# Kernel optimization log

Measured on AMD Instinct MI355X. Metric: run time of the kernel, lower is better.

The kernel has to match this reference:

```python
import jax, jax.numpy as jnp
import numpy as np

# 8 sign-flip operations: all combinations of (+-1, +-1, +-1), shape [8, 3]
OPS = jnp.array([[i, j, k] for i in (-1, 1) for j in (-1, 1) for k in (-1, 1)],
                dtype=jnp.float32)


def setup_inputs() -> dict:
    key = jax.random.key(0)
    k1, k2 = jax.random.split(key)
    B, N = 256, 4096
    X = jax.random.normal(k1, (B, N, 3), dtype=jnp.float32)
    mask = jnp.ones((B, N), dtype=jnp.float32)
    return {"X": X, "mask": mask}


def reference(X, mask):
    # X: [B, N, 3], mask: [B, N]
    m = mask[..., None]                                   # [B, N, 1]
    center = (X * m).sum(axis=1) / m.sum(axis=1)          # [B, 3]
    # torch: X = X - center.unsqueeze(1) * mask  (subtract center only where masked)
    Xc = X - center[:, None, :] * m                       # [B, N, 3]
    # 3x3 covariance per batch element
    C = jnp.einsum('bpi,bpj->bij', Xc, Xc)                # [B, 3, 3]
    # eigh on detached covariance (no grad through eigendecomposition)
    L, V = jnp.linalg.eigh(jax.lax.stop_gradient(C))      # V: [B, 3, 3]
    # F_ops[b,o,i,j] = ops[o,j] * V[b,i,j]  -> [B, 8, 3, 3]
    F_ops = OPS[None, :, None, :] * V[:, None, :, :]
    # h[b,o,p,i] = sum_j F_ops[b,o,j,i] * Xc[b,p,j]
    h = jnp.einsum('boji,bpj->bopi', F_ops, Xc)           # [B, 8, N, 3]
    h = h.reshape(X.shape[0] * 8, X.shape[1], 3)          # [B*8, N, 3]
    return h, jax.lax.stop_gradient(F_ops), center
```

## Files before the change

kernel.cpp:

```cpp
#include <hip/hip_runtime.h>
#include <math.h>

#ifndef USE_NEW_LARTG
#define USE_NEW_LARTG 1
#endif

#define BB 256
#define NN 4096


__device__ __forceinline__ float ssign_(float a, float b) {
  return (b >= 0.0f) ? fabsf(a) : -fabsf(a);
}

__device__ __forceinline__ float slapy2f_(float x, float y) {
#pragma clang fp contract(off)
  float xa = fabsf(x), ya = fabsf(y);
  float w = fmaxf(xa, ya), z = fminf(xa, ya);
  if (z == 0.0f) return w;
  float q = z / w;
  return w * __fsqrt_rn(1.0f + q * q);
}

__device__ __forceinline__ void slartgf_(float f, float g, float& cs, float& sn, float& r) {
#pragma clang fp contract(off)
#if USE_NEW_LARTG
  if (g == 0.0f) { cs = 1.0f; sn = 0.0f; r = f; }
  else if (f == 0.0f) { cs = 0.0f; sn = (g >= 0.0f) ? 1.0f : -1.0f; r = fabsf(g); }
  else {
    float d = __fsqrt_rn(f * f + g * g);
    cs = fabsf(f) / d;
    r = ssign_(d, f);
    sn = g / r;
  }
#else
  if (g == 0.0f) { cs = 1.0f; sn = 0.0f; r = f; }
  else if (f == 0.0f) { cs = 0.0f; sn = 1.0f; r = g; }
  else {
    float rr = __fsqrt_rn(f * f + g * g);
    cs = f / rr; sn = g / rr; r = rr;
    if (fabsf(f) > fabsf(g) && cs < 0.0f) { cs = -cs; sn = -sn; r = -r; }
  }
#endif
}

__device__ __forceinline__ void slaev2f_(float a, float b, float c, float& rt1, float& rt2,
                                         float& cs1, float& sn1) {
#pragma clang fp contract(off)
  float sm = a + c;
  float df = a - c;
  float adf = fabsf(df);
  float tb = b + b;
  float ab = fabsf(tb);
  float acmx, acmn;
  if (fabsf(a) > fabsf(c)) { acmx = a; acmn = c; } else { acmx = c; acmn = a; }
  float rt;
  if (adf > ab)      { float q = ab / adf; rt = adf * __fsqrt_rn(1.0f + q * q); }
  else if (adf < ab) { float q = adf / ab; rt = ab * __fsqrt_rn(1.0f + q * q); }
  else               { rt = ab * __fsqrt_rn(2.0f); }
  int sgn1;
  if (sm < 0.0f)      { rt1 = 0.5f * (sm - rt); sgn1 = -1; rt2 = (acmx / rt1) * acmn - (b / rt1) * b; }
  else if (sm > 0.0f) { rt1 = 0.5f * (sm + rt); sgn1 = 1;  rt2 = (acmx / rt1) * acmn - (b / rt1) * b; }
  else                { rt1 = 0.5f * rt; rt2 = -0.5f * rt; sgn1 = 1; }
  float cs;
  int sgn2;
  if (df >= 0.0f) { cs = df + rt; sgn2 = 1; } else { cs = df - rt; sgn2 = -1; }
  float acs = fabsf(cs);
  if (acs > ab) {
    float ct = -tb / cs;
    sn1 = 1.0f / __fsqrt_rn(1.0f + ct * ct);
    cs1 = ct * sn1;
  } else {
    if (ab == 0.0f) { cs1 = 1.0f; sn1 = 0.0f; }
    else { float tn = -cs / tb; cs1 = 1.0f / __fsqrt_rn(1.0f + tn * tn); sn1 = tn * cs1; }
  }
  if (sgn1 == sgn2) { float tn = cs1; cs1 = -sn1; sn1 = tn; }
}

#define DGET(i)   ((i) == 1 ? d1 : ((i) == 2 ? d2 : d3))
#define DSET(i,v) do { float _t = (v); int _i = (i); \
  d1 = (_i == 1) ? _t : d1; d2 = (_i == 2) ? _t : d2; d3 = (_i == 3) ? _t : d3; } while (0)
#define EGET(i)   ((i) == 1 ? e1 : e2)
#define ESET(i,v) do { float _t = (v); int _i = (i); \
  e1 = (_i == 1) ? _t : e1; e2 = (_i == 2) ? _t : e2; } while (0)
#define WCGET(i)  ((i) == 1 ? wc1 : wc2)
#define WSGET(i)  ((i) == 1 ? ws1 : ws2)
#define WCSET(i,v) do { float _t = (v); int _i = (i); \
  wc1 = (_i == 1) ? _t : wc1; wc2 = (_i == 2) ? _t : wc2; } while (0)
#define WSSET(i,v) do { float _t = (v); int _i = (i); \
  ws1 = (_i == 1) ? _t : ws1; ws2 = (_i == 2) ? _t : ws2; } while (0)
#define ZGETR(rr,j) ((j) == 1 ? z##rr##1 : ((j) == 2 ? z##rr##2 : z##rr##3))
#define ZSETR(rr,j,v) do { float _zv = (v); int _zj = (j); \
  z##rr##1 = (_zj == 1) ? _zv : z##rr##1; \
  z##rr##2 = (_zj == 2) ? _zv : z##rr##2; \
  z##rr##3 = (_zj == 3) ? _zv : z##rr##3; } while (0)
#define ROTR(rr, hi, lo, cc, ss) do { \
  float _zh = ZGETR(rr, (hi)); float _zl = ZGETR(rr, (lo)); \
  float _nh = (cc) * _zh - (ss) * _zl; \
  float _nl = (ss) * _zh + (cc) * _zl; \
  ZSETR(rr, (hi), _nh); ZSETR(rr, (lo), _nl); } while (0)
#define ROTCOLS(hi, lo, cc, ss) do { \
  ROTR(1, hi, lo, cc, ss); ROTR(2, hi, lo, cc, ss); ROTR(3, hi, lo, cc, ss); } while (0)
#define ZSWAPR(rr, i_, k_) do { \
  float _ta = ZGETR(rr, (i_)); float _tb = ZGETR(rr, (k_)); \
  ZSETR(rr, (i_), _tb); ZSETR(rr, (k_), _ta); } while (0)

__device__ __forceinline__ void eigh3_reg(const float C[3][3], float V[3][3]) {
#pragma clang fp contract(off)
  const float eps = 5.9604645e-08f;
  const float eps2 = eps * eps;
  const float safmin = 1.17549435e-38f;
  const int nmaxit = 90;

  float a11 = C[0][0], a21 = C[1][0], a31 = C[2][0];
  float a22 = C[1][1], a32 = C[2][1], a33 = C[2][2];
  float d1, d2, d3, e1, e2, tau1, v3;
  float z11, z12, z13, z21, z22, z23, z31, z32, z33;
  float wc1 = 0.0f, wc2 = 0.0f, ws1 = 0.0f, ws2 = 0.0f;
  int jtot = 0, l1 = 1;
  int m, l, lend, lsv, lendsv, i, j, k, ii;
  float p, g, r, c, s, f, b, rt1, rt2, tst, anorm, cj, sj;

  float xnorm = fabsf(a31);
  if (xnorm == 0.0f) {
    tau1 = 0.0f; v3 = 0.0f;
    d1 = a11; d2 = a22; d3 = a33; e1 = a21; e2 = a32;
  } else {
    float beta = -ssign_(slapy2f_(a21, xnorm), a21);
    tau1 = (beta - a21) / beta;
    v3 = a31 / (a21 - beta);
    e1 = beta;
    float x1 = tau1 * a22 + tau1 * (a32 * v3);
    float x2 = tau1 * a32 + (tau1 * v3) * a33;
    float al = -0.5f * tau1 * (x1 + x2 * v3);
    float w1 = x1 + al;
    float w2 = x2 + al * v3;
    d1 = a11;
    d2 = (a22 - w1) - w1;
    e2 = (a32 - v3 * w1) - w2;
    d3 = (a33 - v3 * w2) - w2 * v3;
  }
  z11 = 1.0f; z12 = 0.0f; z13 = 0.0f;
  z21 = 0.0f; z22 = 1.0f; z23 = 0.0f;
  z31 = 0.0f; z32 = 0.0f; z33 = 1.0f;

L10:
  if (l1 > 3) goto L160;
  if (l1 > 1) ESET(l1 - 1, 0.0f);
  if (l1 <= 2) {
    for (int mm = l1; mm <= 2; ++mm) {
      tst = fabsf(EGET(mm));
      if (tst == 0.0f) { m = mm; goto L30; }
      if (tst <= (__fsqrt_rn(fabsf(DGET(mm))) * __fsqrt_rn(fabsf(DGET(mm + 1)))) * eps) {
        ESET(mm, 0.0f); m = mm; goto L30;
      }
    }
  }
  m = 3;
L30:
  l = l1; lsv = l; lend = m; lendsv = lend; l1 = m + 1;
  if (lend == l) goto L10;
  anorm = 0.0f;
  for (i = l; i <= lend; ++i) anorm = fmaxf(anorm, fabsf(DGET(i)));
  for (i = l; i <= lend - 1; ++i) anorm = fmaxf(anorm, fabsf(EGET(i)));
  if (anorm == 0.0f) goto L10;
  if (fabsf(DGET(lend)) < fabsf(DGET(l))) { lend = lsv; l = lendsv; }

  if (lend > l) {
L40:
    if (l != lend) {
      for (int mm = l; mm <= lend - 1; ++mm) {
        tst = EGET(mm) * EGET(mm);
        if (tst <= (eps2 * fabsf(DGET(mm))) * fabsf(DGET(mm + 1)) + safmin) { m = mm; goto L60; }
      }
    }
    m = lend;
L60:
    if (m < lend) ESET(m, 0.0f);
    p = DGET(l);
    if (m == l) goto L80;
    if (m == l + 1) {
      slaev2f_(DGET(l), EGET(l), DGET(l + 1), rt1, rt2, c, s);
      WCSET(l, c); WSSET(l, s);
      ROTCOLS(l + 1, l, c, s);
      DSET(l, rt1); DSET(l + 1, rt2); ESET(l, 0.0f);
      l = l + 2;
      if (l <= lend) goto L40;
      goto L140;
    }
    if (jtot == nmaxit) goto L140;
    jtot = jtot + 1;
    g = (DGET(l + 1) - p) / (2.0f * EGET(l));
    r = slapy2f_(g, 1.0f);
    g = DGET(m) - p + EGET(l) / (g + ssign_(r, g));
    s = 1.0f; c = 1.0f; p = 0.0f;
    for (i = m - 1; i >= l; --i) {
      f = s * EGET(i); b = c * EGET(i);
      slartgf_(g, f, c, s, r);
      if (i != m - 1) ESET(i + 1, r);
      g = DGET(i + 1) - p;
      r = (DGET(i) - g) * s + 2.0f * c * b;
      p = s * r;
      DSET(i + 1, g + p);
      g = c * r - b;
      WCSET(i, c); WSSET(i, -s);
    }
    for (j = (m - l + 1) - 1; j >= 1; --j) {
      cj = WCGET(l + j - 1); sj = WSGET(l + j - 1);
      ROTCOLS(l + j, l + j - 1, cj, sj);
    }
    DSET(l, DGET(l) - p);
    ESET(l, g);
    goto L40;
L80:
    DSET(l, p);
    l = l + 1;
    if (l <= lend) goto L40;
    goto L140;
  } else {
L90:
    if (l != lend) {
      for (int mm = l; mm >= lend + 1; --mm) {
        tst = EGET(mm - 1) * EGET(mm - 1);
        if (tst <= (eps2 * fabsf(DGET(mm))) * fabsf(DGET(mm - 1)) + safmin) { m = mm; goto L110; }
      }
    }
    m = lend;
L110:
    if (m > lend) ESET(m - 1, 0.0f);
    p = DGET(l);
    if (m == l) goto L130;
    if (m == l - 1) {
      slaev2f_(DGET(l - 1), EGET(l - 1), DGET(l), rt1, rt2, c, s);
      WCSET(m, c); WSSET(m, s);
      ROTCOLS(l, l - 1, c, s);
      DSET(l - 1, rt1); DSET(l, rt2); ESET(l - 1, 0.0f);
      l = l - 2;
      if (l >= lend) goto L90;
      goto L140;
    }
    if (jtot == nmaxit) goto L140;
    jtot = jtot + 1;
    g = (DGET(l - 1) - p) / (2.0f * EGET(l - 1));
    r = slapy2f_(g, 1.0f);
    g = DGET(m) - p + EGET(l - 1) / (g + ssign_(r, g));
    s = 1.0f; c = 1.0f; p = 0.0f;
    for (i = m; i <= l - 1; ++i) {
      f = s * EGET(i); b = c * EGET(i);
      slartgf_(g, f, c, s, r);
      if (i != m) ESET(i - 1, r);
      g = DGET(i) - p;
      r = (DGET(i + 1) - g) * s + 2.0f * c * b;
      p = s * r;
      DSET(i, g + p);
      g = c * r - b;
      WCSET(i, c); WSSET(i, s);
    }
    for (j = 1; j <= (l - m + 1) - 1; ++j) {
      cj = WCGET(m + j - 1); sj = WSGET(m + j - 1);
      ROTCOLS(m + j, m + j - 1, cj, sj);
    }
    DSET(l, DGET(l) - p);
    ESET(l - 1, g);
    goto L90;
L130:
    DSET(l, p);
    l = l - 1;
    if (l >= lend) goto L90;
    goto L140;
  }
L140:
  if (jtot < nmaxit) goto L10;
  goto L190;
L160:
  for (ii = 2; ii <= 3; ++ii) {
    i = ii - 1; k = i; p = DGET(i);
    for (j = ii; j <= 3; ++j) {
      float dj = DGET(j);
      if (dj < p) { k = j; p = dj; }
    }
    if (k != i) {
      DSET(k, DGET(i)); DSET(i, p);
      ZSWAPR(1, i, k); ZSWAPR(2, i, k); ZSWAPR(3, i, k);
    }
  }
L190:
  if (tau1 != 0.0f) {
    float wj, tmp;
    wj = z21 + z31 * v3; tmp = -(tau1 * wj); z21 = z21 + tmp; z31 = z31 + v3 * tmp;
    wj = z22 + z32 * v3; tmp = -(tau1 * wj); z22 = z22 + tmp; z32 = z32 + v3 * tmp;
    wj = z23 + z33 * v3; tmp = -(tau1 * wj); z23 = z23 + tmp; z33 = z33 + v3 * tmp;
  }
  V[0][0] = z11; V[0][1] = z12; V[0][2] = z13;
  V[1][0] = z21; V[1][1] = z22; V[1][2] = z23;
  V[2][0] = z31; V[2][1] = z32; V[2][2] = z33;
}

__global__ __launch_bounds__(256, 4) void k_fused1(
    const float* __restrict__ X, const float* __restrict__ mask,
    float* __restrict__ out_fops, float* __restrict__ out_center,
    float* __restrict__ h) {
  int blk = blockIdx.x;
  int b = blk >> 2;
  int chunk = blk & 3;
  int t = threadIdx.x;

  const float4* Xv = reinterpret_cast<const float4*>(X);
  const float4* Mv = reinterpret_cast<const float4*>(mask);

  double acc[11];
#pragma unroll
  for (int q = 0; q < 11; ++q) acc[q] = 0.0;
  for (int kk = 0; kk < 4; ++kk) {
    int fi = b * 3072 + kk * 768 + 3 * t;
    float4 v0 = Xv[fi], v1 = Xv[fi + 1], v2 = Xv[fi + 2];
    float4 mm = Mv[b * 1024 + kk * 256 + t];
    float px[4] = {v0.x, v0.w, v1.z, v2.y};
    float py[4] = {v0.y, v1.x, v1.w, v2.z};
    float pz[4] = {v0.z, v1.y, v2.x, v2.w};
    float pm[4] = {mm.x, mm.y, mm.z, mm.w};
#pragma unroll
    for (int q = 0; q < 4; ++q) {
      double x = px[q], y = py[q], zz = pz[q], m = pm[q];
      acc[0] += m;       acc[1] += m * m;
      acc[2] += m * x;   acc[3] += m * y;   acc[4] += m * zz;
      acc[5] += x * x;   acc[6] += x * y;   acc[7] += x * zz;
      acc[8] += y * y;   acc[9] += y * zz;  acc[10] += zz * zz;
    }
  }
#pragma unroll
  for (int off = 32; off > 0; off >>= 1)
#pragma unroll
    for (int q = 0; q < 11; ++q) acc[q] += __shfl_down(acc[q], off, 64);

  __shared__ double sh[4][11];
  int wid = t >> 6, lane = t & 63;
  if (lane == 0)
    for (int q = 0; q < 11; ++q) sh[wid][q] = acc[q];
  __syncthreads();

  int fi = b * 3072 + chunk * 768 + 3 * t;
  float4 v0 = Xv[fi], v1 = Xv[fi + 1], v2 = Xv[fi + 2];
  float4 mm = Mv[b * 1024 + chunk * 256 + t];

  __shared__ float svc[12];
  if (t == 0) {
    double r[11];
#pragma unroll
    for (int q = 0; q < 11; ++q)
      r[q] = sh[0][q] + sh[1][q] + sh[2][q] + sh[3][q];
    double W = r[0], W2 = r[1];
    double ssum[3] = {r[2], r[3], r[4]};
    double M[3][3] = {{r[5], r[6], r[7]}, {r[6], r[8], r[9]}, {r[7], r[9], r[10]}};
    double cc[3] = {ssum[0] / W, ssum[1] / W, ssum[2] / W};
    float Cf[3][3];
#pragma unroll
    for (int i = 0; i < 3; ++i)
#pragma unroll
      for (int j = 0; j < 3; ++j)
        Cf[i][j] = (float)(M[i][j] - (ssum[i] * cc[j] + cc[i] * ssum[j]) + W2 * cc[i] * cc[j]);
    float Vf[3][3];
    eigh3_reg(Cf, Vf);
    float cf[3] = {(float)cc[0], (float)cc[1], (float)cc[2]};
#pragma unroll
    for (int i = 0; i < 3; ++i)
#pragma unroll
      for (int j = 0; j < 3; ++j) svc[i * 3 + j] = Vf[i][j];
    svc[9] = cf[0]; svc[10] = cf[1]; svc[11] = cf[2];
    if (chunk == 0) {
      out_center[b * 3 + 0] = cf[0];
      out_center[b * 3 + 1] = cf[1];
      out_center[b * 3 + 2] = cf[2];
#pragma unroll
      for (int o = 0; o < 8; ++o) {
        float sgn[3] = {(o & 4) ? 1.f : -1.f, (o & 2) ? 1.f : -1.f, (o & 1) ? 1.f : -1.f};
#pragma unroll
        for (int i = 0; i < 3; ++i)
#pragma unroll
          for (int j = 0; j < 3; ++j)
            out_fops[b * 72 + o * 9 + i * 3 + j] = sgn[j] * Vf[i][j];
      }
    }
  }
  __syncthreads();

  float V0 = svc[0], V1 = svc[1], V2 = svc[2];
  float V3 = svc[3], V4 = svc[4], V5 = svc[5];
  float V6 = svc[6], V7 = svc[7], V8 = svc[8];
  float c0 = svc[9], c1 = svc[10], c2 = svc[11];

  float px[4] = {v0.x, v0.w, v1.z, v2.y};
  float py[4] = {v0.y, v1.x, v1.w, v2.z};
  float pz[4] = {v0.z, v1.y, v2.x, v2.w};
  float pm[4] = {mm.x, mm.y, mm.z, mm.w};

  float ya[4], yb[4], yc[4];
#pragma unroll
  for (int q = 0; q < 4; ++q) {
    float xcx = px[q] - c0 * pm[q];
    float xcy = py[q] - c1 * pm[q];
    float xcz = pz[q] - c2 * pm[q];
    ya[q] = V0 * xcx + V3 * xcy + V6 * xcz;
    yb[q] = V1 * xcx + V4 * xcy + V7 * xcz;
    yc[q] = V2 * xcx + V5 * xcy + V8 * xcz;
  }

  __shared__ float ylds[3072];
  float4* yv = reinterpret_cast<float4*>(ylds);
  yv[3 * t]     = make_float4(ya[0], yb[0], yc[0], ya[1]);
  yv[3 * t + 1] = make_float4(yb[1], yc[1], ya[2], yb[2]);
  yv[3 * t + 2] = make_float4(yc[2], ya[3], yb[3], yc[3]);
  __syncthreads();

  uint4 r0 = reinterpret_cast<const uint4*>(ylds)[t];
  uint4 r1 = reinterpret_cast<const uint4*>(ylds)[t + 256];
  uint4 r2 = reinterpret_cast<const uint4*>(ylds)[t + 512];

  int c0i = t % 3;
  bool ee0 = (c0i == 0), ee1 = (c0i == 1);

  uint4* hv = reinterpret_cast<uint4*>(h);
  int hb = 3072 * (b * 8) + 768 * chunk;
#pragma unroll
  for (int o = 0; o < 8; ++o) {
    unsigned s0 = (o & 4) ? 0u : 0x80000000u;
    unsigned s1 = (o & 2) ? 0u : 0x80000000u;
    unsigned s2 = (o & 1) ? 0u : 0x80000000u;
    unsigned ma = ee0 ? s0 : (ee1 ? s1 : s2);
    unsigned mb = ee0 ? s1 : (ee1 ? s2 : s0);
    unsigned mc = ee0 ? s2 : (ee1 ? s0 : s1);
    int base = hb + 3072 * o;
    hv[base + t]       = make_uint4(r0.x ^ ma, r0.y ^ mb, r0.z ^ mc, r0.w ^ ma);
    hv[base + t + 256] = make_uint4(r1.x ^ mb, r1.y ^ mc, r1.z ^ ma, r1.w ^ mb);
    hv[base + t + 512] = make_uint4(r2.x ^ mc, r2.y ^ ma, r2.z ^ mb, r2.w ^ mc);
  }
}

extern "C" void kernel_launch(void* const* d_in, const int* in_sizes, int n_in,
                              void* d_out, int out_size, void* d_ws, size_t ws_size,
                              hipStream_t stream) {
  const float* X = (const float*)d_in[0];
  const float* mask = (const float*)d_in[1];
  float* out = (float*)d_out;
  float* h = out;
  float* fops = out + (size_t)BB * 8 * NN * 3;
  float* center = fops + (size_t)BB * 8 * 9;

  hipLaunchKernelGGL(k_fused1, dim3(BB * 4), dim3(256), 0, stream,
                     X, mask, fops, center, h);
}
```

Measured before the change: 33.55 us.

## Use one 1024-thread block per batch to avoid redundant reductions and eigensolves

Replaces four 256-thread blocks per batch element with a single 1024-thread block. Each block reads X and the mask once and runs one reduction and one eigensolve, where before four blocks each re-read the whole batch and repeated the eigensolve. The trade-off is fewer blocks (256 on the device), a serial 16-wave reduction in thread 0, 48KB of LDS per block, and a long single-thread eigh phase that stalls a larger block.

```diff
diff --git a/kernel.cpp b/kernel.cpp
--- a/kernel.cpp
+++ b/kernel.cpp
@@ -296,59 +296,55 @@
   V[2][0] = z31; V[2][1] = z32; V[2][2] = z33;
 }
 
-__global__ __launch_bounds__(256, 4) void k_fused1(
+__global__ __launch_bounds__(1024, 4) void k_fused2(
     const float* __restrict__ X, const float* __restrict__ mask,
     float* __restrict__ out_fops, float* __restrict__ out_center,
     float* __restrict__ h) {
-  int blk = blockIdx.x;
-  int b = blk >> 2;
-  int chunk = blk & 3;
+  int b = blockIdx.x;
   int t = threadIdx.x;
 
   const float4* Xv = reinterpret_cast<const float4*>(X);
   const float4* Mv = reinterpret_cast<const float4*>(mask);
 
+  int fi = b * 3072 + 3 * t;
+  float4 v0 = Xv[fi], v1 = Xv[fi + 1], v2 = Xv[fi + 2];
+  float4 mm = Mv[b * 1024 + t];
+  float px[4] = {v0.x, v0.w, v1.z, v2.y};
+  float py[4] = {v0.y, v1.x, v1.w, v2.z};
+  float pz[4] = {v0.z, v1.y, v2.x, v2.w};
+  float pm[4] = {mm.x, mm.y, mm.z, mm.w};
+
   double acc[11];
 #pragma unroll
   for (int q = 0; q < 11; ++q) acc[q] = 0.0;
-  for (int kk = 0; kk < 4; ++kk) {
-    int fi = b * 3072 + kk * 768 + 3 * t;
-    float4 v0 = Xv[fi], v1 = Xv[fi + 1], v2 = Xv[fi + 2];
-    float4 mm = Mv[b * 1024 + kk * 256 + t];
-    float px[4] = {v0.x, v0.w, v1.z, v2.y};
-    float py[4] = {v0.y, v1.x, v1.w, v2.z};
-    float pz[4] = {v0.z, v1.y, v2.x, v2.w};
-    float pm[4] = {mm.x, mm.y, mm.z, mm.w};
-#pragma unroll
-    for (int q = 0; q < 4; ++q) {
-      double x = px[q], y = py[q], zz = pz[q], m = pm[q];
-      acc[0] += m;       acc[1] += m * m;
-      acc[2] += m * x;   acc[3] += m * y;   acc[4] += m * zz;
-      acc[5] += x * x;   acc[6] += x * y;   acc[7] += x * zz;
-      acc[8] += y * y;   acc[9] += y * zz;  acc[10] += zz * zz;
-    }
+#pragma unroll
+  for (int q = 0; q < 4; ++q) {
+    double x = px[q], y = py[q], zz = pz[q], m = pm[q];
+    acc[0] += m;       acc[1] += m * m;
+    acc[2] += m * x;   acc[3] += m * y;   acc[4] += m * zz;
+    acc[5] += x * x;   acc[6] += x * y;   acc[7] += x * zz;
+    acc[8] += y * y;   acc[9] += y * zz;  acc[10] += zz * zz;
   }
 #pragma unroll
   for (int off = 32; off > 0; off >>= 1)
 #pragma unroll
     for (int q = 0; q < 11; ++q) acc[q] += __shfl_down(acc[q], off, 64);
 
-  __shared__ double sh[4][11];
+  __shared__ double sh[16][11];
   int wid = t >> 6, lane = t & 63;
   if (lane == 0)
     for (int q = 0; q < 11; ++q) sh[wid][q] = acc[q];
   __syncthreads();
 
-  int fi = b * 3072 + chunk * 768 + 3 * t;
-  float4 v0 = Xv[fi], v1 = Xv[fi + 1], v2 = Xv[fi + 2];
-  float4 mm = Mv[b * 1024 + chunk * 256 + t];
-
   __shared__ float svc[12];
   if (t == 0) {
     double r[11];
 #pragma unroll
-    for (int q = 0; q < 11; ++q)
-      r[q] = sh[0][q] + sh[1][q] + sh[2][q] + sh[3][q];
+    for (int q = 0; q < 11; ++q) {
+      double s = 0.0;
+      for (int w = 0; w < 16; ++w) s += sh[w][q];
+      r[q] = s;
+    }
     double W = r[0], W2 = r[1];
     double ssum[3] = {r[2], r[3], r[4]};
     double M[3][3] = {{r[5], r[6], r[7]}, {r[6], r[8], r[9]}, {r[7], r[9], r[10]}};
@@ -367,19 +363,17 @@
 #pragma unroll
       for (int j = 0; j < 3; ++j) svc[i * 3 + j] = Vf[i][j];
     svc[9] = cf[0]; svc[10] = cf[1]; svc[11] = cf[2];
-    if (chunk == 0) {
-      out_center[b * 3 + 0] = cf[0];
-      out_center[b * 3 + 1] = cf[1];
-      out_center[b * 3 + 2] = cf[2];
-#pragma unroll
-      for (int o = 0; o < 8; ++o) {
-        float sgn[3] = {(o & 4) ? 1.f : -1.f, (o & 2) ? 1.f : -1.f, (o & 1) ? 1.f : -1.f};
-#pragma unroll
-        for (int i = 0; i < 3; ++i)
-#pragma unroll
-          for (int j = 0; j < 3; ++j)
-            out_fops[b * 72 + o * 9 + i * 3 + j] = sgn[j] * Vf[i][j];
-      }
+    out_center[b * 3 + 0] = cf[0];
+    out_center[b * 3 + 1] = cf[1];
+    out_center[b * 3 + 2] = cf[2];
+#pragma unroll
+    for (int o = 0; o < 8; ++o) {
+      float sgn[3] = {(o & 4) ? 1.f : -1.f, (o & 2) ? 1.f : -1.f, (o & 1) ? 1.f : -1.f};
+#pragma unroll
+      for (int i = 0; i < 3; ++i)
+#pragma unroll
+        for (int j = 0; j < 3; ++j)
+          out_fops[b * 72 + o * 9 + i * 3 + j] = sgn[j] * Vf[i][j];
     }
   }
   __syncthreads();
@@ -388,11 +382,6 @@
   float V3 = svc[3], V4 = svc[4], V5 = svc[5];
   float V6 = svc[6], V7 = svc[7], V8 = svc[8];
   float c0 = svc[9], c1 = svc[10], c2 = svc[11];
-
-  float px[4] = {v0.x, v0.w, v1.z, v2.y};
-  float py[4] = {v0.y, v1.x, v1.w, v2.z};
-  float pz[4] = {v0.z, v1.y, v2.x, v2.w};
-  float pm[4] = {mm.x, mm.y, mm.z, mm.w};
 
   float ya[4], yb[4], yc[4];
 #pragma unroll
@@ -405,7 +394,7 @@
     yc[q] = V2 * xcx + V5 * xcy + V8 * xcz;
   }
 
-  __shared__ float ylds[3072];
+  __shared__ float ylds[12288];
   float4* yv = reinterpret_cast<float4*>(ylds);
   yv[3 * t]     = make_float4(ya[0], yb[0], yc[0], ya[1]);
   yv[3 * t + 1] = make_float4(yb[1], yc[1], ya[2], yb[2]);
@@ -413,14 +402,14 @@
   __syncthreads();
 
   uint4 r0 = reinterpret_cast<const uint4*>(ylds)[t];
-  uint4 r1 = reinterpret_cast<const uint4*>(ylds)[t + 256];
-  uint4 r2 = reinterpret_cast<const uint4*>(ylds)[t + 512];
+  uint4 r1 = reinterpret_cast<const uint4*>(ylds)[t + 1024];
+  uint4 r2 = reinterpret_cast<const uint4*>(ylds)[t + 2048];
 
   int c0i = t % 3;
   bool ee0 = (c0i == 0), ee1 = (c0i == 1);
 
   uint4* hv = reinterpret_cast<uint4*>(h);
-  int hb = 3072 * (b * 8) + 768 * chunk;
+  int hb = 3072 * (b * 8);
 #pragma unroll
   for (int o = 0; o < 8; ++o) {
     unsigned s0 = (o & 4) ? 0u : 0x80000000u;
@@ -430,9 +419,9 @@
     unsigned mb = ee0 ? s1 : (ee1 ? s2 : s0);
     unsigned mc = ee0 ? s2 : (ee1 ? s0 : s1);
     int base = hb + 3072 * o;
-    hv[base + t]       = make_uint4(r0.x ^ ma, r0.y ^ mb, r0.z ^ mc, r0.w ^ ma);
-    hv[base + t + 256] = make_uint4(r1.x ^ mb, r1.y ^ mc, r1.z ^ ma, r1.w ^ mb);
-    hv[base + t + 512] = make_uint4(r2.x ^ mc, r2.y ^ ma, r2.z ^ mb, r2.w ^ mc);
+    hv[base + t]        = make_uint4(r0.x ^ ma, r0.y ^ mb, r0.z ^ mc, r0.w ^ ma);
+    hv[base + t + 1024] = make_uint4(r1.x ^ mb, r1.y ^ mc, r1.z ^ ma, r1.w ^ mb);
+    hv[base + t + 2048] = make_uint4(r2.x ^ mc, r2.y ^ ma, r2.z ^ mb, r2.w ^ mc);
   }
 }
 
@@ -446,6 +435,6 @@
   float* fops = out + (size_t)BB * 8 * NN * 3;
   float* center = fops + (size_t)BB * 8 * 9;
 
-  hipLaunchKernelGGL(k_fused1, dim3(BB * 4), dim3(256), 0, stream,
+  hipLaunchKernelGGL(k_fused2, dim3(BB), dim3(1024), 0, stream,
                      X, mask, fops, center, h);
 }
```

New measurement: 35.40 us. 5.5% more time.
